# Kernel tuning notes

Measured on AMD Instinct MI355X. Metric: run time of the kernel, lower is better.

The kernel has to match this reference:

```python
import jax, jax.numpy as jnp
from jax import lax
import numpy as np

K = 48          # dim_embedding_key
PAST = 20
FUT = 40
N = 65536       # total surrounding-agent nodes
E = 1048576     # edges
B = 1           # batch (structurally forced to 1 by the original code)


def conv1d_relu(x, w, b):
    # x: [B, 2, T], w: [K, 2, 3], padding=1 -> relu(Conv1d)
    y = lax.conv_general_dilated(x, w, (1,), ((1, 1),),
                                 dimension_numbers=('NCH', 'OIH', 'NCH'))
    return jax.nn.relu(y + b[None, :, None])


def gru_cell(xt, h, Wih, Whh, bih, bhh):
    gi = xt @ Wih.T + bih
    gh = h @ Whh.T + bhh
    ir, iz, inn = jnp.split(gi, 3, axis=-1)
    hr, hz, hn = jnp.split(gh, 3, axis=-1)
    r = jax.nn.sigmoid(ir + hr)
    z = jax.nn.sigmoid(iz + hz)
    n = jnp.tanh(inn + r * hn)
    return (1 - z) * n + z * h


def gru_last(x, Wih, Whh, bih, bhh):
    # x: [Nb, T, Din]; returns final hidden state [Nb, H] (torch GRU, h0 = 0)
    h0 = jnp.zeros((x.shape[0], Whh.shape[1]), x.dtype)
    def step(h, xt):
        h2 = gru_cell(xt, h, Wih, Whh, bih, bhh)
        return h2, None
    hT, _ = lax.scan(step, h0, jnp.swapaxes(x, 0, 1))
    return hT


def gcn_conv(x, row, col, w, W, b, n):
    # PyG GCNConv(normalize=True): add self loops (weight 1), symmetric norm,
    # x @ W.T, gather at source `row`, scatter-add at target `col`, + bias.
    loop = jnp.arange(n)
    row = jnp.concatenate([row, loop])
    col = jnp.concatenate([col, loop])
    w = jnp.concatenate([w, jnp.ones((n,), w.dtype)])
    deg = jax.ops.segment_sum(w, col, num_segments=n)
    dinv = jnp.where(deg > 0, lax.rsqrt(jnp.where(deg > 0, deg, 1.0)), 0.0)
    norm = dinv[row] * w * dinv[col]
    xw = x @ W.T
    msg = xw[row] * norm[:, None]
    return jax.ops.segment_sum(msg, col, num_segments=n) + b


def forward(past, future, x, edge_index, edge_weight,
            conv_past_w, conv_past_b, conv_fut_w, conv_fut_b,
            enc_past_Wih, enc_past_Whh, enc_past_bih, enc_past_bhh,
            enc_fut_Wih, enc_fut_Whh, enc_fut_bih, enc_fut_bhh,
            dec_Wih, dec_Whh, dec_bih, dec_bhh,
            fc_w, fc_b, gcn1_w, gcn1_b, gcn2_w, gcn2_b):
    present0 = past[:, -1, :2]                                  # [B, 2]

    # --- surrounding agents: conv1d + GRU encoder over all N nodes ---
    inter_past = jnp.swapaxes(x.reshape(-1, PAST, 2), 1, 2)     # [N, 2, T]
    story_embed = jnp.swapaxes(conv1d_relu(inter_past, conv_past_w, conv_past_b), 1, 2)
    state_past = gru_last(story_embed, enc_past_Wih, enc_past_Whh, enc_past_bih, enc_past_bhh)  # [N, K]

    # --- GCN interaction (edge_weight nonempty branch); dropout is eval-mode identity ---
    ei = edge_index.reshape(2, -1)
    ew = edge_weight.reshape(-1)
    x1 = jax.nn.relu(gcn_conv(state_past, ei[0], ei[1], ew, gcn1_w, gcn1_b, N))
    x1 = gcn_conv(x1, ei[0], ei[1], ew, gcn2_w, gcn2_b, N)
    interact_past = x1[0].reshape(B, -1)                        # [B, K] (B == 1)

    # --- ego past / future encoders ---
    past_embed = jnp.swapaxes(conv1d_relu(jnp.swapaxes(past, 1, 2), conv_past_w, conv_past_b), 1, 2)
    fut_embed = jnp.swapaxes(conv1d_relu(jnp.swapaxes(future, 1, 2), conv_fut_w, conv_fut_b), 1, 2)
    target_past = gru_last(past_embed, enc_past_Wih, enc_past_Whh, enc_past_bih, enc_past_bhh)   # [B, K]
    state_fut = gru_last(fut_embed, enc_fut_Wih, enc_fut_Whh, enc_fut_bih, enc_fut_bhh)          # [B, K]

    state_conc = jnp.concatenate([interact_past, target_past, state_fut], axis=-1)               # [B, 3K]

    zeros_in = jnp.zeros_like(state_conc)
    def step(carry, i):
        h, present = carry
        inp = jnp.where(i == 0, state_conc, zeros_in)
        h = gru_cell(inp, h, dec_Wih, dec_Whh, dec_bih, dec_bhh)
        coords = present + h @ fc_w.T + fc_b
        return (h, coords), coords
    (_, _), coords_seq = lax.scan(step, (jnp.zeros((B, 3 * K), past.dtype), present0), jnp.arange(FUT))
    return jnp.swapaxes(coords_seq, 0, 1)                        # [B, FUT, 2]


def setup_inputs() -> dict:
    ks = jax.random.split(jax.random.key(0), 32)
    def p(k, shape, s=0.1):
        return jax.random.normal(k, shape, jnp.float32) * s
    inp = {
        'past': p(ks[0], (B, PAST, 2), 1.0),
        'future': p(ks[1], (B, FUT, 2), 1.0),
        'x': p(ks[2], (N, PAST, 2), 1.0),
        'edge_index': jax.random.randint(ks[3], (1, 2, E), 0, N, jnp.int32),
        'edge_weight': jax.random.uniform(ks[4], (1, E), jnp.float32),
        'conv_past_w': p(ks[5], (K, 2, 3)), 'conv_past_b': p(ks[6], (K,)),
        'conv_fut_w': p(ks[7], (K, 2, 3)), 'conv_fut_b': p(ks[8], (K,)),
        'enc_past_Wih': p(ks[9], (3 * K, K)), 'enc_past_Whh': p(ks[10], (3 * K, K)),
        'enc_past_bih': p(ks[11], (3 * K,)), 'enc_past_bhh': p(ks[12], (3 * K,)),
        'enc_fut_Wih': p(ks[13], (3 * K, K)), 'enc_fut_Whh': p(ks[14], (3 * K, K)),
        'enc_fut_bih': p(ks[15], (3 * K,)), 'enc_fut_bhh': p(ks[16], (3 * K,)),
        'dec_Wih': p(ks[17], (9 * K, 3 * K)), 'dec_Whh': p(ks[18], (9 * K, 3 * K)),
        'dec_bih': p(ks[19], (9 * K,)), 'dec_bhh': p(ks[20], (9 * K,)),
        'fc_w': p(ks[21], (2, 3 * K)), 'fc_b': p(ks[22], (2,)),
        'gcn1_w': p(ks[23], (K, K)), 'gcn1_b': p(ks[24], (K,)),
        'gcn2_w': p(ks[25], (K, K)), 'gcn2_b': p(ks[26], (K,)),
    }
    return inp


def reference(past, future, x, edge_index, edge_weight,
              conv_past_w, conv_past_b, conv_fut_w, conv_fut_b,
              enc_past_Wih, enc_past_Whh, enc_past_bih, enc_past_bhh,
              enc_fut_Wih, enc_fut_Whh, enc_fut_bih, enc_fut_bhh,
              dec_Wih, dec_Whh, dec_bih, dec_bhh,
              fc_w, fc_b, gcn1_w, gcn1_b, gcn2_w, gcn2_b):
    return forward(past, future, x, edge_index, edge_weight,
                   conv_past_w, conv_past_b, conv_fut_w, conv_fut_b,
                   enc_past_Wih, enc_past_Whh, enc_past_bih, enc_past_bhh,
                   enc_fut_Wih, enc_fut_Whh, enc_fut_bih, enc_fut_bhh,
                   dec_Wih, dec_Whh, dec_bih, dec_bhh,
                   fc_w, fc_b, gcn1_w, gcn1_b, gcn2_w, gcn2_b)
```

## Files before the change

### kernel.cpp

```cpp
#include <hip/hip_runtime.h>
#include <math.h>

#define NN 65536
#define NE 1048576
#define KH 48
#define G3 144
#define DEGB 512

#define CAP_L1 8192
#define CAP_S1 4096
#define CAP_E2 65536
#define CAP_S2 8192

#define OFF_MARK1  0u
#define OFF_MARK2  262144u
#define OFF_CNT    524288u
#define OFF_L1R    524352u
#define OFF_L1W    557120u
#define OFF_S1G    589888u
#define OFF_E2R    606272u
#define OFF_E2S    868416u
#define OFF_E2W    1130560u
#define OFF_S2     1392704u
#define OFF_DEG2   1425472u
#define OFF_STATE  1458240u
#define OFF_X1     3031104u
#define OFF_TPSF   3817536u
#define OFF_WHH16  3818048u
#define OFF_GI0P   3942464u

typedef _Float16 h2_t __attribute__((ext_vector_type(2)));
typedef _Float16 h4_t __attribute__((ext_vector_type(4)));

__device__ __forceinline__ float sigmf(float x) { return 1.0f / (1.0f + expf(-x)); }

#if __has_builtin(__builtin_amdgcn_fdot2)
__device__ __forceinline__ float fdot2f(h2_t a, h2_t b, float c) {
    return __builtin_amdgcn_fdot2(a, b, c, false);
}
#else
__device__ __forceinline__ float fdot2f(h2_t a, h2_t b, float c) {
    return c + (float)a.x * (float)b.x + (float)a.y * (float)b.y;
}
#endif

__global__ void k_edges1(const int* ei, const float* ew,
                         int* mark1, unsigned* cnt, int* l1r, float* l1w) {
    int q = blockIdx.x * blockDim.x + threadIdx.x;
    if (q >= NE / 4) return;
    if (q == 0) mark1[0] = 1;
    int4 c4 = reinterpret_cast<const int4*>(ei + NE)[q];
    int e = q * 4;
    int cc[4] = {c4.x, c4.y, c4.z, c4.w};
#pragma unroll
    for (int j = 0; j < 4; ++j) {
        if (cc[j] == 0) {
            int r = ei[e + j];
            float w = ew[e + j];
            unsigned s = atomicAdd(&cnt[0], 1u);
            if (s < CAP_L1) { l1r[s] = r; l1w[s] = w; }
            mark1[r] = 1;
        }
    }
}

__global__ void k_compact1(int* mark1, int* mark2, unsigned* cnt,
                           int* e2r, int* e2s, float* e2w, int* s1g,
                           float* x1, const float* g1b) {
    int i = blockIdx.x * blockDim.x + threadIdx.x;
    if (i >= NN) return;
    if (mark1[i]) {
        unsigned s = atomicAdd(&cnt[1], 1u);
        if (s < CAP_S1) {
            mark1[i] = (int)s + 1;
            mark2[i] = 1;
            s1g[s] = i;
            unsigned t = atomicAdd(&cnt[2], 1u);
            if (t < CAP_E2) { e2r[t] = i; e2s[t] = (int)s; e2w[t] = 1.0f; }
            for (int k = 0; k < KH; ++k) x1[s * KH + k] = g1b[k];
        } else {
            mark1[i] = 0;
        }
    }
}

__global__ void k_edges2(const int* ei, const float* ew,
                         const int* mark1, int* mark2, unsigned* cnt,
                         int* e2r, int* e2s, float* e2w) {
    int q = blockIdx.x * blockDim.x + threadIdx.x;
    if (q >= NE / 4) return;
    int4 c4 = reinterpret_cast<const int4*>(ei + NE)[q];
    int e = q * 4;
    int cc[4] = {c4.x, c4.y, c4.z, c4.w};
#pragma unroll
    for (int j = 0; j < 4; ++j) {
        int m = mark1[cc[j]];
        if (m > 0) {
            int r = ei[e + j];
            float w = ew[e + j];
            unsigned s = atomicAdd(&cnt[2], 1u);
            if (s < CAP_E2) { e2r[s] = r; e2s[s] = m - 1; e2w[s] = w; }
            mark2[r] = 1;
        }
    }
}

__global__ void k_compact2(int* mark2, unsigned* cnt, int* s2, float* deg2) {
    int i = blockIdx.x * blockDim.x + threadIdx.x;
    if (i >= NN) return;
    if (mark2[i]) {
        unsigned s = atomicAdd(&cnt[3], 1u);
        if (s < CAP_S2) { s2[s] = i; mark2[i] = (int)s + 1; deg2[s] = 1.0f; }
        else mark2[i] = 0;
    }
}

__device__ void gru_seq(const float* xseq, int T,
                        const float* cw, const float* cb,
                        const float* Wih, const float* Whh,
                        const float* bih, const float* bhh,
                        float* out48,
                        float* s_x, float* s_embed, float* s_giA,
                        float* s_h ) {
    int t = threadIdx.x;
    int nt = blockDim.x;
    for (int i = t; i < T * 2; i += nt) s_x[i] = xseq[i];
    __syncthreads();
    for (int idx = t; idx < T * KH; idx += nt) {
        int tt = idx / KH;
        int k = idx - tt * KH;
        float acc = cb[k];
#pragma unroll
        for (int d = 0; d < 3; ++d) {
            int tau = tt + d - 1;
            if (tau >= 0 && tau < T) {
                acc += cw[k * 6 + d] * s_x[tau * 2 + 0];
                acc += cw[k * 6 + 3 + d] * s_x[tau * 2 + 1];
            }
        }
        s_embed[tt * KH + k] = fmaxf(acc, 0.0f);
    }
    __syncthreads();
    for (int idx = t; idx < T * G3; idx += nt) {
        int step = idx / G3;
        int row = idx - step * G3;
        const float4* wp = reinterpret_cast<const float4*>(Wih + row * KH);
        const float4* em = reinterpret_cast<const float4*>(s_embed + step * KH);
        float g = bih[row];
#pragma unroll
        for (int j = 0; j < 12; ++j) {
            float4 w4 = wp[j]; float4 e4 = em[j];
            g += w4.x * e4.x + w4.y * e4.y + w4.z * e4.z + w4.w * e4.w;
        }
        s_giA[idx] = g;
    }
    int k = t >> 1, hf = t & 1;
    float4 wr[18];
    float bh0 = 0.0f, bh1 = 0.0f, bh2 = 0.0f;
    if (t < 96) {
#pragma unroll
        for (int g = 0; g < 3; ++g) {
            const float4* q = reinterpret_cast<const float4*>(
                Whh + (g * KH + k) * KH + hf * 24);
#pragma unroll
            for (int j = 0; j < 6; ++j) wr[g * 6 + j] = q[j];
        }
        if (hf == 0) { bh0 = bhh[k]; bh1 = bhh[KH + k]; bh2 = bhh[2 * KH + k]; }
    }
    if (t < KH) s_h[t] = 0.0f;
    float hk = 0.0f;
    for (int step = 0; step < T; ++step) {
        __syncthreads();
        int cur = step & 1, nxt = cur ^ 1;
        if (t < 96) {
            const float4* hp = reinterpret_cast<const float4*>(s_h + cur * KH)
                               + hf * 6;
            float a0 = bh0, a1 = bh1, a2 = bh2;
#pragma unroll
            for (int j = 0; j < 6; ++j) {
                float4 hv = hp[j];
                float4 w0 = wr[j], w1 = wr[6 + j], w2 = wr[12 + j];
                a0 += w0.x * hv.x + w0.y * hv.y + w0.z * hv.z + w0.w * hv.w;
                a1 += w1.x * hv.x + w1.y * hv.y + w1.z * hv.z + w1.w * hv.w;
                a2 += w2.x * hv.x + w2.y * hv.y + w2.z * hv.z + w2.w * hv.w;
            }
            a0 += __shfl_xor(a0, 1);
            a1 += __shfl_xor(a1, 1);
            a2 += __shfl_xor(a2, 1);
            if (hf == 0) {
                const float* gi = s_giA + step * G3;
                float r = sigmf(gi[k] + a0);
                float z = sigmf(gi[KH + k] + a1);
                float n = tanhf(gi[2 * KH + k] + r * a2);
                hk = (1.0f - z) * n + z * hk;
                s_h[nxt * KH + k] = hk;
            }
        }
    }
    __syncthreads();
    if (t < KH) out48[t] = s_h[(T & 1) * KH + t];
}

__global__ __launch_bounds__(192, 2) void k_gru(
    const float* x, const float* cpw, const float* cpb,
    const float* epWih, const float* epWhh, const float* epbih, const float* epbhh,
    const float* cfw, const float* cfb,
    const float* efWih, const float* efWhh, const float* efbih, const float* efbhh,
    const float* past, const float* future,
    const int* ei, const float* ew, const int* mark2, float* deg2,
    const int* s2, const unsigned* cnt, float* state, float* tpsf) {
    if (blockIdx.x < DEGB) {
        int per = NE / DEGB;
        int lo = blockIdx.x * per;
        for (int e = lo + threadIdx.x; e < lo + per; e += blockDim.x) {
            int c = ei[NE + e];
            int m = mark2[c];
            if (m > 0) atomicAdd(&deg2[m - 1], ew[e]);
        }
        return;
    }
    __shared__ __align__(16) float s_x[80];
    __shared__ __align__(16) float s_embed[40 * KH];
    __shared__ __align__(16) float s_giA[40 * G3];
    __shared__ __align__(16) float s_h[2 * KH];
    if (blockIdx.x == DEGB) {
        gru_seq(past, 20, cpw, cpb, epWih, epWhh, epbih, epbhh,
                tpsf, s_x, s_embed, s_giA, s_h);
        return;
    }
    if (blockIdx.x == DEGB + 1) {
        gru_seq(future, 40, cfw, cfb, efWih, efWhh, efbih, efbhh,
                tpsf + 64, s_x, s_embed, s_giA, s_h);
        return;
    }
    int b0 = blockIdx.x - (DEGB + 2);
    int nw = gridDim.x - (DEGB + 2);
    int cnt2 = (int)min(cnt[3], (unsigned)CAP_S2);
    for (int b = b0; b < cnt2; b += nw) {
        int node = s2[b];
        gru_seq(x + (size_t)node * 40, 20, cpw, cpb, epWih, epWhh, epbih, epbhh,
                state + (size_t)b * KH, s_x, s_embed, s_giA, s_h);
    }
}

__global__ void k_acc1(const unsigned* cnt, const int* e2r, const int* e2s,
                       const float* e2w, const int* mark2, const float* deg2,
                       const int* s1g, const float* state,
                       const float* W1, float* x1,
                       const float* dWhh, const float* dWih,
                       const float* dbih, const float* tpsf,
                       _Float16* whh16, float* gi0p) {
    if (blockIdx.x < 64) {
        int id = blockIdx.x * blockDim.x + threadIdx.x;
        if (id < 27 * 576) {
            int c = id / 576, t = id - c * 576;
            int k = t >> 2, q = t & 3;
            int g = c / 9, u = c - g * 9;
            const float* src = dWhh + (size_t)(g * G3 + k) * G3 + q * 36 + 4 * u;
            float4 f = *reinterpret_cast<const float4*>(src);
            h2_t a, b;
            a.x = (_Float16)f.x; a.y = (_Float16)f.y;
            b.x = (_Float16)f.z; b.y = (_Float16)f.w;
            h2_t* o = reinterpret_cast<h2_t*>(whh16);
            o[2 * id + 0] = a;
            o[2 * id + 1] = b;
            return;
        }
        int row = id - 27 * 576;
        if (row < 432) {
            const float* wr = dWih + (size_t)row * G3;
            float acc = dbih[row];
#pragma unroll
            for (int m = 0; m < 48; ++m) acc += wr[48 + m] * tpsf[m];
#pragma unroll
            for (int m = 0; m < 48; ++m) acc += wr[96 + m] * tpsf[64 + m];
            gi0p[row] = acc;
        }
        return;
    }
    int nE = (int)min(cnt[2], (unsigned)CAP_E2);
    int total = nE * KH;
    int stride = (gridDim.x - 64) * blockDim.x;
    for (int idx = (blockIdx.x - 64) * blockDim.x + threadIdx.x; idx < total;
         idx += stride) {
        int e = idx / KH;
        int k = idx - e * KH;
        int row = e2r[e];
        int s2i = mark2[row] - 1;
        if (s2i < 0) continue;
        int cglob = s1g[e2s[e]];
        int cs2 = mark2[cglob] - 1;
        float norm = e2w[e] * rsqrtf(deg2[s2i] * deg2[cs2]);
        const float* sp = state + (size_t)s2i * KH;
        const float* wp = W1 + k * KH;
        float acc = 0.0f;
#pragma unroll
        for (int m = 0; m < KH; ++m) acc += sp[m] * wp[m];
        atomicAdd(&x1[e2s[e] * KH + k], acc * norm);
    }
}

__global__ __launch_bounds__(640, 1) void k_dec(
    const unsigned* cnt, const int* l1r, const float* l1w,
    const int* mark1, const int* mark2, const float* deg2, const float* x1,
    const float* W2, const float* b2, const float* tpsf, const float* past,
    const float* dWih, const _Float16* whh16, const float* gi0p,
    const float* dbih, const float* dbhh,
    const float* fcw, const float* fcb, float* out) {
    __shared__ __align__(16) float s_conc[G3];
    __shared__ __align__(16) _Float16 s_h16[2][G3];
    __shared__ __align__(16) float s_hf[2][G3];
    int t = threadIdx.x;
    if (t < 48) s_conc[t] = b2[t];
    else if (t < 96) s_conc[t] = tpsf[t - 48];
    else if (t < 144) s_conc[t] = tpsf[64 + t - 96];
    if (t < G3) {
        s_h16[0][t] = (_Float16)0.0f;
        s_hf[0][t] = 0.0f;
    }
    __syncthreads();
    int cl1 = (int)min(cnt[0], (unsigned)CAP_L1);
    float dinv0 = rsqrtf(deg2[mark2[0] - 1]);
    int items = (cl1 + 1) * KH;
    for (int idx = t; idx < items; idx += blockDim.x) {
        int e = idx / KH;
        int k = idx - e * KH;
        int row; float norm;
        if (e == cl1) { row = 0; norm = dinv0 * dinv0; }
        else {
            row = l1r[e];
            int rs2 = mark2[row] - 1;
            if (rs2 < 0) continue;
            norm = l1w[e] * rsqrtf(deg2[rs2]) * dinv0;
        }
        int s1 = mark1[row] - 1;
        if (s1 < 0) continue;
        const float* xp = x1 + (size_t)s1 * KH;
        const float* wp = W2 + k * KH;
        float acc = 0.0f;
#pragma unroll
        for (int m = 0; m < KH; ++m) acc += fmaxf(xp[m], 0.0f) * wp[m];
        atomicAdd(&s_conc[k], acc * norm);
    }
    int k = t >> 2, q = t & 3;
    h2_t wh[54];
    float bh[3] = {0.0f, 0.0f, 0.0f};
    float bi[3] = {0.0f, 0.0f, 0.0f};
    if (t < 576) {
        const h4_t* wp = reinterpret_cast<const h4_t*>(whh16);
#pragma unroll
        for (int c = 0; c < 27; ++c) {
            h4_t v = wp[c * 576 + t];
            wh[2 * c] = __builtin_shufflevector(v, v, 0, 1);
            wh[2 * c + 1] = __builtin_shufflevector(v, v, 2, 3);
        }
        if (q == 0) {
#pragma unroll
            for (int g = 0; g < 3; ++g) {
                bh[g] = dbhh[g * G3 + k];
                bi[g] = dbih[g * G3 + k];
            }
        }
    }
    float fw0[3] = {0, 0, 0}, fw1[3] = {0, 0, 0};
    float fcb0 = 0.0f, fcb1 = 0.0f, pres0 = 0.0f, pres1 = 0.0f;
    if (t >= 576) {
        int lane = t - 576;
#pragma unroll
        for (int j = 0; j < 3; ++j) {
            int m = lane + 64 * j;
            if (m < G3) { fw0[j] = fcw[m]; fw1[j] = fcw[G3 + m]; }
        }
        if (lane == 0) {
            fcb0 = fcb[0]; fcb1 = fcb[1];
            pres0 = past[38]; pres1 = past[39];
        }
    }
    __syncthreads();
    float gi0[3] = {0.0f, 0.0f, 0.0f};
    if (t < 576) {
#pragma unroll
        for (int g = 0; g < 3; ++g) {
            float acc = 0.0f;
            if (q == 0) {
                const float4* p = reinterpret_cast<const float4*>(
                    dWih + (size_t)(g * G3 + k) * G3);
                const float4* cc = reinterpret_cast<const float4*>(s_conc);
#pragma unroll
                for (int j = 0; j < 9; ++j) {
                    float4 w4 = p[j]; float4 c4 = cc[j];
                    acc += w4.x * c4.x + w4.y * c4.y + w4.z * c4.z + w4.w * c4.w;
                }
            } else if (q == 1) {
                const float4* p = reinterpret_cast<const float4*>(
                    dWih + (size_t)(g * G3 + k) * G3 + 36);
                const float4* cc = reinterpret_cast<const float4*>(s_conc + 36);
#pragma unroll
                for (int j = 0; j < 3; ++j) {
                    float4 w4 = p[j]; float4 c4 = cc[j];
                    acc += w4.x * c4.x + w4.y * c4.y + w4.z * c4.z + w4.w * c4.w;
                }
            }
            acc += __shfl_xor(acc, 1);
            acc += __shfl_xor(acc, 2);
            gi0[g] = acc + gi0p[g * G3 + k];
        }
    }
    float hk = 0.0f;
    for (int i = 0; i < 40; ++i) {
        __syncthreads();
        int cur = i & 1, nxt = cur ^ 1;
        if (t < 576) {
            const h4_t* hp = reinterpret_cast<const h4_t*>(&s_h16[cur][0]) + q * 9;
            float a0 = bh[0], a1 = bh[1], a2 = bh[2];
#pragma unroll
            for (int j = 0; j < 9; ++j) {
                h4_t hv = hp[j];
                h2_t lo = __builtin_shufflevector(hv, hv, 0, 1);
                h2_t hi = __builtin_shufflevector(hv, hv, 2, 3);
                a0 = fdot2f(wh[2 * j], lo, a0);
                a1 = fdot2f(wh[18 + 2 * j], lo, a1);
                a2 = fdot2f(wh[36 + 2 * j], lo, a2);
                a0 = fdot2f(wh[2 * j + 1], hi, a0);
                a1 = fdot2f(wh[18 + 2 * j + 1], hi, a1);
                a2 = fdot2f(wh[36 + 2 * j + 1], hi, a2);
            }
            a0 += __shfl_xor(a0, 1); a0 += __shfl_xor(a0, 2);
            a1 += __shfl_xor(a1, 1); a1 += __shfl_xor(a1, 2);
            a2 += __shfl_xor(a2, 1); a2 += __shfl_xor(a2, 2);
            if (q == 0) {
                float gr = ((i == 0) ? gi0[0] : bi[0]) + a0;
                float gz = ((i == 0) ? gi0[1] : bi[1]) + a1;
                float gn = ((i == 0) ? gi0[2] : bi[2]);
                float r = sigmf(gr);
                float z = sigmf(gz);
                float n = tanhf(gn + r * a2);
                hk = (1.0f - z) * n + z * hk;
                s_h16[nxt][k] = (_Float16)hk;
                s_hf[nxt][k] = hk;
            }
        } else if (i >= 1) {
            int lane = t - 576;
            const float* hsrc = s_hf[cur];
            float p0 = 0.0f, p1 = 0.0f;
#pragma unroll
            for (int j = 0; j < 3; ++j) {
                int m = lane + 64 * j;
                if (m < G3) { float h = hsrc[m]; p0 += h * fw0[j]; p1 += h * fw1[j]; }
            }
#pragma unroll
            for (int off = 32; off > 0; off >>= 1) {
                p0 += __shfl_down(p0, off);
                p1 += __shfl_down(p1, off);
            }
            if (lane == 0) {
                pres0 += p0 + fcb0; pres1 += p1 + fcb1;
                out[(i - 1) * 2 + 0] = pres0;
                out[(i - 1) * 2 + 1] = pres1;
            }
        }
    }
    __syncthreads();
    if (t >= 576) {
        int lane = t - 576;
        const float* hsrc = s_hf[0];
        float p0 = 0.0f, p1 = 0.0f;
#pragma unroll
        for (int j = 0; j < 3; ++j) {
            int m = lane + 64 * j;
            if (m < G3) { float h = hsrc[m]; p0 += h * fw0[j]; p1 += h * fw1[j]; }
        }
#pragma unroll
        for (int off = 32; off > 0; off >>= 1) {
            p0 += __shfl_down(p0, off);
            p1 += __shfl_down(p1, off);
        }
        if (lane == 0) {
            pres0 += p0 + fcb0; pres1 += p1 + fcb1;
            out[39 * 2 + 0] = pres0;
            out[39 * 2 + 1] = pres1;
        }
    }
}

extern "C" void kernel_launch(void* const* d_in, const int* in_sizes, int n_in,
                              void* d_out, int out_size, void* d_ws, size_t ws_size,
                              hipStream_t stream) {
    (void)in_sizes; (void)n_in; (void)out_size; (void)ws_size;
    const float* past   = (const float*)d_in[0];
    const float* future = (const float*)d_in[1];
    const float* x      = (const float*)d_in[2];
    const int*   ei     = (const int*)d_in[3];
    const float* ew     = (const float*)d_in[4];
    const float* cpw    = (const float*)d_in[5];
    const float* cpb    = (const float*)d_in[6];
    const float* cfw    = (const float*)d_in[7];
    const float* cfb    = (const float*)d_in[8];
    const float* epWih  = (const float*)d_in[9];
    const float* epWhh  = (const float*)d_in[10];
    const float* epbih  = (const float*)d_in[11];
    const float* epbhh  = (const float*)d_in[12];
    const float* efWih  = (const float*)d_in[13];
    const float* efWhh  = (const float*)d_in[14];
    const float* efbih  = (const float*)d_in[15];
    const float* efbhh  = (const float*)d_in[16];
    const float* dWih   = (const float*)d_in[17];
    const float* dWhh   = (const float*)d_in[18];
    const float* dbih   = (const float*)d_in[19];
    const float* dbhh   = (const float*)d_in[20];
    const float* fcw    = (const float*)d_in[21];
    const float* fcb    = (const float*)d_in[22];
    const float* g1w    = (const float*)d_in[23];
    const float* g1b    = (const float*)d_in[24];
    const float* g2w    = (const float*)d_in[25];
    const float* g2b    = (const float*)d_in[26];

    char* ws = (char*)d_ws;
    int*      mark1 = (int*)(ws + OFF_MARK1);
    int*      mark2 = (int*)(ws + OFF_MARK2);
    unsigned* cnt   = (unsigned*)(ws + OFF_CNT);
    int*      l1r   = (int*)(ws + OFF_L1R);
    float*    l1w   = (float*)(ws + OFF_L1W);
    int*      s1g   = (int*)(ws + OFF_S1G);
    int*      e2r   = (int*)(ws + OFF_E2R);
    int*      e2s   = (int*)(ws + OFF_E2S);
    float*    e2w   = (float*)(ws + OFF_E2W);
    int*      s2    = (int*)(ws + OFF_S2);
    float*    deg2  = (float*)(ws + OFF_DEG2);
    float*    state = (float*)(ws + OFF_STATE);
    float*    x1    = (float*)(ws + OFF_X1);
    float*    tpsf  = (float*)(ws + OFF_TPSF);
    _Float16* whh16 = (_Float16*)(ws + OFF_WHH16);
    float*    gi0p  = (float*)(ws + OFF_GI0P);

    hipMemsetAsync(ws, 0, 524352, stream);
    k_edges1<<<NE / 4 / 256, 256, 0, stream>>>(ei, ew, mark1, cnt, l1r, l1w);
    k_compact1<<<NN / 256, 256, 0, stream>>>(mark1, mark2, cnt, e2r, e2s, e2w, s1g, x1, g1b);
    k_edges2<<<NE / 4 / 256, 256, 0, stream>>>(ei, ew, mark1, mark2, cnt, e2r, e2s, e2w);
    k_compact2<<<NN / 256, 256, 0, stream>>>(mark2, cnt, s2, deg2);
    k_gru<<<DEGB + 2 + 512, 192, 0, stream>>>(x, cpw, cpb, epWih, epWhh, epbih, epbhh,
                                              cfw, cfb, efWih, efWhh, efbih, efbhh,
                                              past, future, ei, ew, mark2, deg2,
                                              s2, cnt, state, tpsf);
    k_acc1<<<64 + 128, 256, 0, stream>>>(cnt, e2r, e2s, e2w, mark2, deg2, s1g,
                                         state, g1w, x1,
                                         dWhh, dWih, dbih, tpsf, whh16, gi0p);
    k_dec<<<1, 640, 0, stream>>>(cnt, l1r, l1w, mark1, mark2, deg2, x1, g2w, g2b,
                                 tpsf, past, dWih, whh16, gi0p, dbih, dbhh, fcw, fcb,
                                 (float*)d_out);
}
```

Baseline: 241.9 us.

## Precompute ego past/future conv and input-gate projections in edge-scan kernel

Adds 15 extra blocks to the first edge-scan kernel. They compute the conv1d embedding and input-gate projection (Wih·x + bih) for the ego agent's past and future sequences ahead of time and write them to workspace. The two dedicated GRU blocks in k_gru then only run the hidden-state recurrence from these precomputed gates, which shortens their serial critical path. In exchange the edge kernel gains extra blocks and the GRU blocks read the gates from global memory.

Measured after the change: 224.7 us. -7.1%, faster.

```diff
diff --git a/kernel.cpp b/kernel.cpp
--- a/kernel.cpp
+++ b/kernel.cpp
@@ -6,6 +6,7 @@
 #define KH 48
 #define G3 144
 #define DEGB 512
+#define PREPB 15
 
 #define CAP_L1 8192
 #define CAP_S1 4096
@@ -28,6 +29,8 @@
 #define OFF_TPSF   3817536u
 #define OFF_WHH16  3818048u
 #define OFF_GI0P   3942464u
+#define OFF_GIP    3944192u
+#define OFF_GIF    3955712u
 
 typedef _Float16 h2_t __attribute__((ext_vector_type(2)));
 typedef _Float16 h4_t __attribute__((ext_vector_type(4)));
@@ -45,7 +48,58 @@
 #endif
 
 __global__ void k_edges1(const int* ei, const float* ew,
-                         int* mark1, unsigned* cnt, int* l1r, float* l1w) {
+                         int* mark1, unsigned* cnt, int* l1r, float* l1w,
+                         const float* past, const float* future,
+                         const float* cpw, const float* cpb,
+                         const float* cfw, const float* cfb,
+                         const float* epWih, const float* epbih,
+                         const float* efWih, const float* efbih,
+                         float* giP, float* giF) {
+    if (blockIdx.x >= NE / 4 / 256) {
+        int p = blockIdx.x - NE / 4 / 256;
+        const float* xs; const float* cw; const float* cb;
+        const float* Wih; const float* bih; float* gout;
+        int T, s0;
+        if (p < 5) { xs = past;   cw = cpw; cb = cpb; Wih = epWih; bih = epbih;
+                     gout = giP; T = 20; s0 = p * 4; }
+        else       { xs = future; cw = cfw; cb = cfb; Wih = efWih; bih = efbih;
+                     gout = giF; T = 40; s0 = (p - 5) * 4; }
+        __shared__ __align__(16) float s_x[80];
+        __shared__ __align__(16) float s_e[4 * KH];
+        int t = threadIdx.x;
+        if (t < T * 2) s_x[t] = xs[t];
+        __syncthreads();
+        for (int idx = t; idx < 4 * KH; idx += 256) {
+            int lt = idx / KH;
+            int k = idx - lt * KH;
+            int tt = s0 + lt;
+            float acc = cb[k];
+#pragma unroll
+            for (int d = 0; d < 3; ++d) {
+                int tau = tt + d - 1;
+                if (tau >= 0 && tau < T) {
+                    acc += cw[k * 6 + d] * s_x[tau * 2 + 0];
+                    acc += cw[k * 6 + 3 + d] * s_x[tau * 2 + 1];
+                }
+            }
+            s_e[lt * KH + k] = fmaxf(acc, 0.0f);
+        }
+        __syncthreads();
+        for (int idx = t; idx < 4 * G3; idx += 256) {
+            int lt = idx / G3;
+            int row = idx - lt * G3;
+            const float4* wp = reinterpret_cast<const float4*>(Wih + row * KH);
+            const float4* em = reinterpret_cast<const float4*>(s_e + lt * KH);
+            float g = bih[row];
+#pragma unroll
+            for (int j = 0; j < 12; ++j) {
+                float4 w4 = wp[j]; float4 e4 = em[j];
+                g += w4.x * e4.x + w4.y * e4.y + w4.z * e4.z + w4.w * e4.w;
+            }
+            gout[(s0 + lt) * G3 + row] = g;
+        }
+        return;
+    }
     int q = blockIdx.x * blockDim.x + threadIdx.x;
     if (q >= NE / 4) return;
     if (q == 0) mark1[0] = 1;
@@ -201,12 +255,62 @@
     if (t < KH) out48[t] = s_h[(T & 1) * KH + t];
 }
 
+__device__ void gru_rec(const float* giA , int T,
+                        const float* Whh, const float* bhh,
+                        float* out48, float* s_h ) {
+    int t = threadIdx.x;
+    int k = t >> 1, hf = t & 1;
+    float4 wr[18];
+    float bh0 = 0.0f, bh1 = 0.0f, bh2 = 0.0f;
+    if (t < 96) {
+#pragma unroll
+        for (int g = 0; g < 3; ++g) {
+            const float4* q = reinterpret_cast<const float4*>(
+                Whh + (g * KH + k) * KH + hf * 24);
+#pragma unroll
+            for (int j = 0; j < 6; ++j) wr[g * 6 + j] = q[j];
+        }
+        if (hf == 0) { bh0 = bhh[k]; bh1 = bhh[KH + k]; bh2 = bhh[2 * KH + k]; }
+    }
+    if (t < KH) s_h[t] = 0.0f;
+    float hk = 0.0f;
+    for (int step = 0; step < T; ++step) {
+        __syncthreads();
+        int cur = step & 1, nxt = cur ^ 1;
+        if (t < 96) {
+            const float4* hp = reinterpret_cast<const float4*>(s_h + cur * KH)
+                               + hf * 6;
+            float a0 = bh0, a1 = bh1, a2 = bh2;
+#pragma unroll
+            for (int j = 0; j < 6; ++j) {
+                float4 hv = hp[j];
+                float4 w0 = wr[j], w1 = wr[6 + j], w2 = wr[12 + j];
+                a0 += w0.x * hv.x + w0.y * hv.y + w0.z * hv.z + w0.w * hv.w;
+                a1 += w1.x * hv.x + w1.y * hv.y + w1.z * hv.z + w1.w * hv.w;
+                a2 += w2.x * hv.x + w2.y * hv.y + w2.z * hv.z + w2.w * hv.w;
+            }
+            a0 += __shfl_xor(a0, 1);
+            a1 += __shfl_xor(a1, 1);
+            a2 += __shfl_xor(a2, 1);
+            if (hf == 0) {
+                const float* gi = giA + step * G3;
+                float r = sigmf(gi[k] + a0);
+                float z = sigmf(gi[KH + k] + a1);
+                float n = tanhf(gi[2 * KH + k] + r * a2);
+                hk = (1.0f - z) * n + z * hk;
+                s_h[nxt * KH + k] = hk;
+            }
+        }
+    }
+    __syncthreads();
+    if (t < KH) out48[t] = s_h[(T & 1) * KH + t];
+}
+
 __global__ __launch_bounds__(192, 2) void k_gru(
     const float* x, const float* cpw, const float* cpb,
     const float* epWih, const float* epWhh, const float* epbih, const float* epbhh,
-    const float* cfw, const float* cfb,
-    const float* efWih, const float* efWhh, const float* efbih, const float* efbhh,
-    const float* past, const float* future,
+    const float* efWhh, const float* efbhh,
+    const float* giP, const float* giF,
     const int* ei, const float* ew, const int* mark2, float* deg2,
     const int* s2, const unsigned* cnt, float* state, float* tpsf) {
     if (blockIdx.x < DEGB) {
@@ -224,13 +328,11 @@
     __shared__ __align__(16) float s_giA[40 * G3];
     __shared__ __align__(16) float s_h[2 * KH];
     if (blockIdx.x == DEGB) {
-        gru_seq(past, 20, cpw, cpb, epWih, epWhh, epbih, epbhh,
-                tpsf, s_x, s_embed, s_giA, s_h);
+        gru_rec(giP, 20, epWhh, epbhh, tpsf, s_h);
         return;
     }
     if (blockIdx.x == DEGB + 1) {
-        gru_seq(future, 40, cfw, cfb, efWih, efWhh, efbih, efbhh,
-                tpsf + 64, s_x, s_embed, s_giA, s_h);
+        gru_rec(giF, 40, efWhh, efbhh, tpsf + 64, s_h);
         return;
     }
     int b0 = blockIdx.x - (DEGB + 2);
@@ -532,15 +634,20 @@
     float*    tpsf  = (float*)(ws + OFF_TPSF);
     _Float16* whh16 = (_Float16*)(ws + OFF_WHH16);
     float*    gi0p  = (float*)(ws + OFF_GI0P);
+    float*    giP   = (float*)(ws + OFF_GIP);
+    float*    giF   = (float*)(ws + OFF_GIF);
 
     hipMemsetAsync(ws, 0, 524352, stream);
-    k_edges1<<<NE / 4 / 256, 256, 0, stream>>>(ei, ew, mark1, cnt, l1r, l1w);
+    k_edges1<<<NE / 4 / 256 + PREPB, 256, 0, stream>>>(
+        ei, ew, mark1, cnt, l1r, l1w,
+        past, future, cpw, cpb, cfw, cfb,
+        epWih, epbih, efWih, efbih, giP, giF);
     k_compact1<<<NN / 256, 256, 0, stream>>>(mark1, mark2, cnt, e2r, e2s, e2w, s1g, x1, g1b);
     k_edges2<<<NE / 4 / 256, 256, 0, stream>>>(ei, ew, mark1, mark2, cnt, e2r, e2s, e2w);
     k_compact2<<<NN / 256, 256, 0, stream>>>(mark2, cnt, s2, deg2);
     k_gru<<<DEGB + 2 + 512, 192, 0, stream>>>(x, cpw, cpb, epWih, epWhh, epbih, epbhh,
-                                              cfw, cfb, efWih, efWhh, efbih, efbhh,
-                                              past, future, ei, ew, mark2, deg2,
+                                              efWhh, efbhh, giP, giF,
+                                              ei, ew, mark2, deg2,
                                               s2, cnt, state, tpsf);
     k_acc1<<<64 + 128, 256, 0, stream>>>(cnt, e2r, e2s, e2w, mark2, deg2, s1g,
                                          state, g1w, x1,
```
